# Kernel optimization log

Measured on AMD Instinct MI355X. Metric: run time of the kernel, lower is better.

## Reference

```python
import jax, jax.numpy as jnp
import numpy as np

N_NODES = 100000
N_EDGES = 1600000
D = 64
BN_EPS = 1e-5


def setup_inputs() -> dict:
    key = jax.random.key(0)
    ks = jax.random.split(key, 10)
    s = 1.0 / np.sqrt(D)
    return {
        "features": jax.random.normal(ks[0], (N_NODES, D), dtype=jnp.float32),
        "src": jax.random.randint(ks[1], (N_EDGES,), 0, N_NODES, dtype=jnp.int32),
        "dst": jax.random.randint(ks[2], (N_EDGES,), 0, N_NODES, dtype=jnp.int32),
        "eps": jnp.zeros((), dtype=jnp.float32),
        "W1": jax.random.uniform(ks[3], (D, D), jnp.float32, -s, s),
        "b1": jax.random.uniform(ks[4], (D,), jnp.float32, -s, s),
        "W2": jax.random.uniform(ks[5], (D, D), jnp.float32, -s, s),
        "b2": jax.random.uniform(ks[6], (D,), jnp.float32, -s, s),
        "gamma": jnp.ones((D,), dtype=jnp.float32),
        "beta": jnp.zeros((D,), dtype=jnp.float32),
    }


def reference(features, src, dst, eps, W1, b1, W2, b2, gamma, beta):
    h_in = features
    # message passing: gather src node features, scatter-sum to dst (fn.copy_u + fn.sum)
    neigh = jax.ops.segment_sum(features[src], dst, num_segments=N_NODES)  # [N, D]
    # eps-weighted self term
    h = (1.0 + eps) * features + neigh
    # apply_func MLP: Linear -> ReLU -> Linear
    h = jnp.maximum(h @ W1 + b1, 0.0) @ W2 + b2
    # BatchNorm1d over nodes (training-mode batch statistics)
    mean = jnp.mean(h, axis=0)
    var = jnp.var(h, axis=0)
    h = (h - mean) * jax.lax.rsqrt(var + BN_EPS) * gamma + beta
    # activation
    h = jnp.maximum(h, 0.0)
    # residual (indim == outdim)
    h = h_in + h
    # dropout p=0 -> identity
    return h
```

## Files before the change

kernel.cpp:

```cpp
#include <hip/hip_runtime.h>
#include <hip/hip_fp16.h>

#define N_NODES 100000
#define N_EDGES 1600000
#define D 64
#define BN_EPS 1e-5f
#define NBKT 256
#define NPB 391
#define BKT_CAP 7680
#define SORT_T 1024
#define NSHARD 64

typedef _Float16 half8 __attribute__((ext_vector_type(8)));
typedef float f32x4 __attribute__((ext_vector_type(4)));

__global__ __launch_bounds__(256) void bucket_k(
    const int* __restrict__ src, const int* __restrict__ dst,
    int* __restrict__ bkt_cnt, int2* __restrict__ bktbuf)
{
    __shared__ int h[NBKT], base[NBKT], cur[NBKT];
    const int t = threadIdx.x;
    if (t < NBKT) { h[t] = 0; cur[t] = 0; }
    __syncthreads();
    const int e0 = blockIdx.x * 4096;
    int s[16], d[16], b[16];
    #pragma unroll
    for (int i = 0; i < 16; ++i) {
        int e = e0 + i * 256 + t;
        if (e < N_EDGES) {
            s[i] = src[e];
            d[i] = dst[e];
            b[i] = d[i] / NPB;
            atomicAdd(&h[b[i]], 1);
        } else {
            b[i] = -1;
        }
    }
    __syncthreads();
    if (t < NBKT) base[t] = atomicAdd(&bkt_cnt[t], h[t]);
    __syncthreads();
    #pragma unroll
    for (int i = 0; i < 16; ++i) {
        if (b[i] >= 0) {
            int p = atomicAdd(&cur[b[i]], 1);
            bktbuf[(size_t)b[i] * BKT_CAP + base[b[i]] + p] = make_int2(s[i], d[i]);
        }
    }
}

__global__ __launch_bounds__(SORT_T) void sort_k(
    const int2* __restrict__ bktbuf, const int* __restrict__ bkt_cnt,
    int* __restrict__ rowptr, int* __restrict__ col)
{
    __shared__ int h[NPB];
    __shared__ int cur[NPB];
    __shared__ int part[SORT_T];
    __shared__ int bsc[NBKT];

    const int b = blockIdx.x;
    const int t = threadIdx.x;
    const int nb0 = b * NPB;
    const int nodes_in = min(NPB, N_NODES - nb0);
    const int cnt = bkt_cnt[b];
    const int2* buf = bktbuf + (size_t)b * BKT_CAP;

    if (t < NBKT) bsc[t] = bkt_cnt[t];
    __syncthreads();
    for (int off = 1; off < NBKT; off <<= 1) {
        int x = 0;
        if (t < NBKT) {
            x = bsc[t];
            if (t >= off) x += bsc[t - off];
        }
        __syncthreads();
        if (t < NBKT) bsc[t] = x;
        __syncthreads();
    }
    const int gbase = bsc[b] - cnt;

    if (t < NPB) h[t] = 0;
    __syncthreads();

    for (int i = t; i < cnt; i += SORT_T)
        atomicAdd(&h[buf[i].y - nb0], 1);
    __syncthreads();

    int a = (t < NPB) ? h[t] : 0;
    part[t] = a;
    __syncthreads();
    for (int off = 1; off < SORT_T; off <<= 1) {
        int x = part[t];
        int u = (t >= off) ? part[t - off] : 0;
        __syncthreads();
        part[t] = x + u;
        __syncthreads();
    }
    int excl = part[t] - a;
    if (t < NPB) {
        cur[t] = excl;
        if (t < nodes_in) rowptr[nb0 + t] = gbase + excl;
    }
    if (b == NBKT - 1 && t == 0) rowptr[N_NODES] = N_EDGES;
    __syncthreads();

    for (int i = t; i < cnt; i += SORT_T) {
        int2 r = buf[i];
        int slot = atomicAdd(&cur[r.y - nb0], 1);
        col[gbase + slot] = r.x;
    }
}

__global__ __launch_bounds__(256) void conv_k(
    const float* __restrict__ feat, __half* __restrict__ feat16)
{
    size_t i = ((size_t)blockIdx.x * 256 + threadIdx.x) * 8;
    if (i < (size_t)N_NODES * D) {
        float4 v0 = *(const float4*)(feat + i);
        float4 v1 = *(const float4*)(feat + i + 4);
        __half2 o[4];
        o[0] = __floats2half2_rn(v0.x, v0.y);
        o[1] = __floats2half2_rn(v0.z, v0.w);
        o[2] = __floats2half2_rn(v1.x, v1.y);
        o[3] = __floats2half2_rn(v1.z, v1.w);
        *(float4*)(feat16 + i) = *(float4*)o;
    }
}

__global__ __launch_bounds__(256) void wprep_k(
    const float* __restrict__ W1, const float* __restrict__ W2,
    _Float16* __restrict__ w1t, _Float16* __restrict__ w2t)
{
    const int t = threadIdx.x;
    const int n = t >> 2;
    const int k0 = (t & 3) * 16;
    _Float16 o1[16], o2[16];
    #pragma unroll
    for (int j = 0; j < 16; ++j) {
        o1[j] = (_Float16)W1[(k0 + j) * 64 + n];
        o2[j] = (_Float16)W2[(k0 + j) * 64 + n];
    }
    #pragma unroll
    for (int j = 0; j < 16; j += 8) {
        *(half8*)(w1t + n * 64 + k0 + j) = *(half8*)&o1[j];
        *(half8*)(w2t + n * 64 + k0 + j) = *(half8*)&o2[j];
    }
}

__global__ __launch_bounds__(256) void gather16_k(
    const __half* __restrict__ feat16, const int* __restrict__ rowptr,
    const int* __restrict__ col, const float* __restrict__ epsp,
    __half* __restrict__ x16)
{
    int node = blockIdx.x * 4 + (threadIdx.x >> 6);
    int lane = threadIdx.x & 63;
    if (node >= N_NODES) return;
    int g = lane >> 3;
    int c = (lane & 7) << 3;
    int lo = rowptr[node];
    int hi = rowptr[node + 1];
    float a[8] = {0.f, 0.f, 0.f, 0.f, 0.f, 0.f, 0.f, 0.f};
    int e = lo + g;
    for (; e + 8 < hi; e += 16) {
        int s0 = col[e];
        int s1 = col[e + 8];
        float4 r0 = *(const float4*)(feat16 + (size_t)s0 * D + c);
        float4 r1 = *(const float4*)(feat16 + (size_t)s1 * D + c);
        const __half2* h0 = (const __half2*)&r0;
        const __half2* h1 = (const __half2*)&r1;
        #pragma unroll
        for (int i = 0; i < 4; ++i) {
            float2 f0 = __half22float2(h0[i]);
            float2 f1 = __half22float2(h1[i]);
            a[2 * i]     += f0.x + f1.x;
            a[2 * i + 1] += f0.y + f1.y;
        }
    }
    if (e < hi) {
        float4 r0 = *(const float4*)(feat16 + (size_t)col[e] * D + c);
        const __half2* h0 = (const __half2*)&r0;
        #pragma unroll
        for (int i = 0; i < 4; ++i) {
            float2 f0 = __half22float2(h0[i]);
            a[2 * i]     += f0.x;
            a[2 * i + 1] += f0.y;
        }
    }
    #pragma unroll
    for (int off = 8; off <= 32; off <<= 1)
        #pragma unroll
        for (int i = 0; i < 8; ++i)
            a[i] += __shfl_xor(a[i], off, 64);
    if (g == 0) {
        float4 rs = *(const float4*)(feat16 + (size_t)node * D + c);
        const __half2* hs = (const __half2*)&rs;
        const float epsv = 1.0f + epsp[0];
        __half2 o[4];
        #pragma unroll
        for (int i = 0; i < 4; ++i) {
            float2 fs = __half22float2(hs[i]);
            o[i] = __floats2half2_rn(fmaf(epsv, fs.x, a[2 * i]),
                                     fmaf(epsv, fs.y, a[2 * i + 1]));
        }
        *(float4*)(x16 + (size_t)node * D + c) = *(float4*)o;
    }
}

__global__ __launch_bounds__(256) void gather32_k(
    const float* __restrict__ feat, const int* __restrict__ rowptr,
    const int* __restrict__ col, const float* __restrict__ epsp,
    float* __restrict__ x)
{
    int node = blockIdx.x * 4 + (threadIdx.x >> 6);
    int lane = threadIdx.x & 63;
    if (node >= N_NODES) return;
    int g = lane >> 4;
    int c = (lane & 15) << 2;
    int lo = rowptr[node];
    int hi = rowptr[node + 1];
    float ax = 0.f, ay = 0.f, az = 0.f, aw = 0.f;
    int e = lo + g;
    for (; e + 4 < hi; e += 8) {
        int s0 = col[e];
        int s1 = col[e + 4];
        float4 v0 = *(const float4*)(feat + (size_t)s0 * D + c);
        float4 v1 = *(const float4*)(feat + (size_t)s1 * D + c);
        ax += v0.x; ay += v0.y; az += v0.z; aw += v0.w;
        ax += v1.x; ay += v1.y; az += v1.z; aw += v1.w;
    }
    if (e < hi) {
        float4 v = *(const float4*)(feat + (size_t)col[e] * D + c);
        ax += v.x; ay += v.y; az += v.z; aw += v.w;
    }
    #pragma unroll
    for (int off = 16; off <= 32; off <<= 1) {
        ax += __shfl_xor(ax, off, 64);
        ay += __shfl_xor(ay, off, 64);
        az += __shfl_xor(az, off, 64);
        aw += __shfl_xor(aw, off, 64);
    }
    if (g == 0) {
        float4 f = *(const float4*)(feat + (size_t)node * D + c);
        const float epsv = 1.0f + epsp[0];
        float4 r;
        r.x = fmaf(epsv, f.x, ax);
        r.y = fmaf(epsv, f.y, ay);
        r.z = fmaf(epsv, f.z, az);
        r.w = fmaf(epsv, f.w, aw);
        *(float4*)(x + (size_t)node * D + c) = r;
    }
}

__global__ __launch_bounds__(256) void mfma_mlp2_k(
    const __half* __restrict__ x16,
    const _Float16* __restrict__ w1t, const _Float16* __restrict__ w2t,
    const float* __restrict__ b1, const float* __restrict__ b2,
    __half* __restrict__ h216, float* __restrict__ stats)
{
    __shared__ __align__(16) _Float16 xts[64 * 72];

    const int t    = threadIdx.x;
    const int w    = t >> 6;
    const int lane = t & 63;
    const int m    = lane & 15;
    const int q    = lane >> 4;
    const int rbase = w * 16;
    const int nb   = blockIdx.x * 64;

    const _Float16* xg = (const _Float16*)x16 + (size_t)(nb + rbase + m) * 64 + q * 8;
    half8 a0 = *(const half8*)(xg);
    half8 a1 = *(const half8*)(xg + 32);

    f32x4 acc[4];
    #pragma unroll
    for (int jt = 0; jt < 4; ++jt) {
        const float bias = b1[jt * 16 + m];
        acc[jt] = (f32x4){bias, bias, bias, bias};
        const _Float16* bw = w1t + (jt * 16 + m) * 64 + q * 8;
        half8 bf0 = *(const half8*)(bw);
        half8 bf1 = *(const half8*)(bw + 32);
        acc[jt] = __builtin_amdgcn_mfma_f32_16x16x32_f16(a0, bf0, acc[jt], 0, 0, 0);
        acc[jt] = __builtin_amdgcn_mfma_f32_16x16x32_f16(a1, bf1, acc[jt], 0, 0, 0);
    }

    #pragma unroll
    for (int jt = 0; jt < 4; ++jt)
        #pragma unroll
        for (int r = 0; r < 4; ++r)
            xts[(rbase + q * 4 + r) * 72 + jt * 16 + m] =
                (_Float16)fmaxf(acc[jt][r], 0.0f);
    asm volatile("s_waitcnt lgkmcnt(0)" ::: "memory");

    const _Float16* xw = &xts[(rbase + m) * 72 + q * 8];
    half8 c0 = *(const half8*)(xw);
    half8 c1 = *(const half8*)(xw + 32);

    f32x4 acc2[4];
    #pragma unroll
    for (int jt = 0; jt < 4; ++jt) {
        const float bias = b2[jt * 16 + m];
        acc2[jt] = (f32x4){bias, bias, bias, bias};
        const _Float16* bw = w2t + (jt * 16 + m) * 64 + q * 8;
        half8 bf0 = *(const half8*)(bw);
        half8 bf1 = *(const half8*)(bw + 32);
        acc2[jt] = __builtin_amdgcn_mfma_f32_16x16x32_f16(c0, bf0, acc2[jt], 0, 0, 0);
        acc2[jt] = __builtin_amdgcn_mfma_f32_16x16x32_f16(c1, bf1, acc2[jt], 0, 0, 0);
    }
    asm volatile("s_waitcnt lgkmcnt(0)" ::: "memory");

    float psums[4], psqs[4];
    #pragma unroll
    for (int jt = 0; jt < 4; ++jt) {
        float ps = 0.f, pq = 0.f;
        #pragma unroll
        for (int r = 0; r < 4; ++r) {
            const int row = rbase + q * 4 + r;
            const float v = acc2[jt][r];
            const float vv = (nb + row < N_NODES) ? v : 0.f;
            ps += vv;
            pq += vv * vv;
            xts[row * 72 + jt * 16 + m] = (_Float16)v;
        }
        ps += __shfl_xor(ps, 16, 64); ps += __shfl_xor(ps, 32, 64);
        pq += __shfl_xor(pq, 16, 64); pq += __shfl_xor(pq, 32, 64);
        psums[jt] = ps; psqs[jt] = pq;
    }
    if (lane < 16) {
        float* sp = stats + (size_t)(blockIdx.x & (NSHARD - 1)) * 128;
        #pragma unroll
        for (int jt = 0; jt < 4; ++jt) {
            unsafeAtomicAdd(sp + jt * 16 + lane,      psums[jt]);
            unsafeAtomicAdd(sp + 64 + jt * 16 + lane, psqs[jt]);
        }
    }
    asm volatile("s_waitcnt lgkmcnt(0)" ::: "memory");

    {
        const int rr = lane >> 2;
        const int cc = (lane & 3) * 16;
        const int gn = nb + rbase + rr;
        if (gn < N_NODES) {
            float4 r0 = *(const float4*)&xts[(rbase + rr) * 72 + cc];
            float4 r1 = *(const float4*)&xts[(rbase + rr) * 72 + cc + 8];
            *(float4*)(h216 + (size_t)gn * 64 + cc)     = r0;
            *(float4*)(h216 + (size_t)gn * 64 + cc + 8) = r1;
        }
    }
}

__global__ __launch_bounds__(256) void mlp32_k(
    const float* __restrict__ x,
    const float* __restrict__ W1, const float* __restrict__ b1,
    const float* __restrict__ W2, const float* __restrict__ b2,
    float* __restrict__ h2out, float* __restrict__ stats)
{
    __shared__ float W1s[64 * 68];
    __shared__ float W2s[64 * 68];
    __shared__ float xs[64 * 65];
    __shared__ float b1s[64], b2s[64];

    const int t  = threadIdx.x;
    const int nb = blockIdx.x * 64;

    #pragma unroll
    for (int i = 0; i < 4; ++i) {
        int l  = t + i * 256;
        int k  = l >> 4;
        int j4 = (l & 15) << 2;
        *(float4*)(&W1s[k * 68 + j4]) = *(const float4*)(W1 + k * 64 + j4);
        *(float4*)(&W2s[k * 68 + j4]) = *(const float4*)(W2 + k * 64 + j4);
    }
    if (t < 64)       b1s[t]      = b1[t];
    else if (t < 128) b2s[t - 64] = b2[t - 64];

    #pragma unroll
    for (int i = 0; i < 2; ++i) {
        int n  = (t >> 3) + i * 32;
        int k8 = (t & 7) << 3;
        int gn = nb + n;
        float4 a = make_float4(0.f, 0.f, 0.f, 0.f), b = a;
        if (gn < N_NODES) {
            a = *(const float4*)(x + (size_t)gn * D + k8);
            b = *(const float4*)(x + (size_t)gn * D + k8 + 4);
        }
        *(float4*)&xs[n * 65 + k8]     = a;
        *(float4*)&xs[n * 65 + k8 + 4] = b;
    }
    __syncthreads();

    const int n0 = (t & 15) << 2;
    const int j0 = (t >> 4) << 2;
    const float* xr0 = &xs[(n0 + 0) * 65];
    const float* xr1 = &xs[(n0 + 1) * 65];
    const float* xr2 = &xs[(n0 + 2) * 65];
    const float* xr3 = &xs[(n0 + 3) * 65];

    float acc[4][4];
    #pragma unroll
    for (int a = 0; a < 4; ++a)
        #pragma unroll
        for (int b = 0; b < 4; ++b)
            acc[a][b] = b1s[j0 + b];

    #pragma unroll 8
    for (int k = 0; k < 64; ++k) {
        const float4 w = *(const float4*)(&W1s[k * 68 + j0]);
        const float x0 = xr0[k], x1 = xr1[k], x2 = xr2[k], x3 = xr3[k];
        acc[0][0] = fmaf(x0, w.x, acc[0][0]); acc[0][1] = fmaf(x0, w.y, acc[0][1]);
        acc[0][2] = fmaf(x0, w.z, acc[0][2]); acc[0][3] = fmaf(x0, w.w, acc[0][3]);
        acc[1][0] = fmaf(x1, w.x, acc[1][0]); acc[1][1] = fmaf(x1, w.y, acc[1][1]);
        acc[1][2] = fmaf(x1, w.z, acc[1][2]); acc[1][3] = fmaf(x1, w.w, acc[1][3]);
        acc[2][0] = fmaf(x2, w.x, acc[2][0]); acc[2][1] = fmaf(x2, w.y, acc[2][1]);
        acc[2][2] = fmaf(x2, w.z, acc[2][2]); acc[2][3] = fmaf(x2, w.w, acc[2][3]);
        acc[3][0] = fmaf(x3, w.x, acc[3][0]); acc[3][1] = fmaf(x3, w.y, acc[3][1]);
        acc[3][2] = fmaf(x3, w.z, acc[3][2]); acc[3][3] = fmaf(x3, w.w, acc[3][3]);
    }

    __syncthreads();
    #pragma unroll
    for (int a = 0; a < 4; ++a)
        #pragma unroll
        for (int b = 0; b < 4; ++b)
            xs[(n0 + a) * 65 + j0 + b] = fmaxf(acc[a][b], 0.0f);
    __syncthreads();

    float acc2[4][4];
    #pragma unroll
    for (int a = 0; a < 4; ++a)
        #pragma unroll
        for (int b = 0; b < 4; ++b)
            acc2[a][b] = b2s[j0 + b];

    #pragma unroll 8
    for (int k = 0; k < 64; ++k) {
        const float4 w = *(const float4*)(&W2s[k * 68 + j0]);
        const float x0 = xr0[k], x1 = xr1[k], x2 = xr2[k], x3 = xr3[k];
        acc2[0][0] = fmaf(x0, w.x, acc2[0][0]); acc2[0][1] = fmaf(x0, w.y, acc2[0][1]);
        acc2[0][2] = fmaf(x0, w.z, acc2[0][2]); acc2[0][3] = fmaf(x0, w.w, acc2[0][3]);
        acc2[1][0] = fmaf(x1, w.x, acc2[1][0]); acc2[1][1] = fmaf(x1, w.y, acc2[1][1]);
        acc2[1][2] = fmaf(x1, w.z, acc2[1][2]); acc2[1][3] = fmaf(x1, w.w, acc2[1][3]);
        acc2[2][0] = fmaf(x2, w.x, acc2[2][0]); acc2[2][1] = fmaf(x2, w.y, acc2[2][1]);
        acc2[2][2] = fmaf(x2, w.z, acc2[2][2]); acc2[2][3] = fmaf(x2, w.w, acc2[2][3]);
        acc2[3][0] = fmaf(x3, w.x, acc2[3][0]); acc2[3][1] = fmaf(x3, w.y, acc2[3][1]);
        acc2[3][2] = fmaf(x3, w.z, acc2[3][2]); acc2[3][3] = fmaf(x3, w.w, acc2[3][3]);
    }

    float psum[4] = {0.f, 0.f, 0.f, 0.f};
    float psq[4]  = {0.f, 0.f, 0.f, 0.f};
    #pragma unroll
    for (int a = 0; a < 4; ++a) {
        int gn = nb + n0 + a;
        if (gn < N_NODES) {
            float4 hh;
            hh.x = acc2[a][0]; hh.y = acc2[a][1]; hh.z = acc2[a][2]; hh.w = acc2[a][3];
            *(float4*)(h2out + (size_t)gn * 64 + j0) = hh;
            psum[0] += hh.x; psq[0] += hh.x * hh.x;
            psum[1] += hh.y; psq[1] += hh.y * hh.y;
            psum[2] += hh.z; psq[2] += hh.z * hh.z;
            psum[3] += hh.w; psq[3] += hh.w * hh.w;
        }
    }
    #pragma unroll
    for (int off = 8; off >= 1; off >>= 1)
        #pragma unroll
        for (int b = 0; b < 4; ++b) {
            psum[b] += __shfl_down(psum[b], off, 16);
            psq[b]  += __shfl_down(psq[b],  off, 16);
        }
    if ((t & 15) == 0) {
        float* sp = stats + (size_t)(blockIdx.x & (NSHARD - 1)) * 128;
        #pragma unroll
        for (int b = 0; b < 4; ++b) {
            unsafeAtomicAdd(sp + j0 + b,      psum[b]);
            unsafeAtomicAdd(sp + 64 + j0 + b, psq[b]);
        }
    }
}

__global__ void bnstats_k(const float* __restrict__ stats,
                          const float* __restrict__ gamma,
                          const float* __restrict__ beta,
                          float* __restrict__ sf)
{
    int j = threadIdx.x;
    float s = 0.f, q = 0.f;
    for (int c = 0; c < NSHARD; ++c) {
        s += stats[c * 128 + j];
        q += stats[c * 128 + 64 + j];
    }
    const float invN = 1.0f / (float)N_NODES;
    float mean  = s * invN;
    float var   = q * invN - mean * mean;
    float scale = gamma[j] * rsqrtf(var + BN_EPS);
    sf[j]      = scale;
    sf[64 + j] = beta[j] - mean * scale;
}

__global__ __launch_bounds__(256) void finish16_k(
    const float* __restrict__ feat, const __half* __restrict__ h216,
    const float* __restrict__ sf, float* __restrict__ out)
{
    __shared__ float scs[64], shs[64];
    if (threadIdx.x < 64) {
        scs[threadIdx.x] = sf[threadIdx.x];
        shs[threadIdx.x] = sf[64 + threadIdx.x];
    }
    __syncthreads();
    size_t i = (size_t)blockIdx.x * 256 + threadIdx.x;
    if (i < (size_t)N_NODES * D / 4) {
        int j = (int)((i * 4) & 63);
        const __half2* hp = (const __half2*)(h216 + i * 4);
        float2 h0 = __half22float2(hp[0]);
        float2 h1 = __half22float2(hp[1]);
        float4 f = *(const float4*)(feat + i * 4);
        float4 o;
        o.x = fmaxf(fmaf(h0.x, scs[j + 0], shs[j + 0]), 0.f) + f.x;
        o.y = fmaxf(fmaf(h0.y, scs[j + 1], shs[j + 1]), 0.f) + f.y;
        o.z = fmaxf(fmaf(h1.x, scs[j + 2], shs[j + 2]), 0.f) + f.z;
        o.w = fmaxf(fmaf(h1.y, scs[j + 3], shs[j + 3]), 0.f) + f.w;
        *(float4*)(out + i * 4) = o;
    }
}

__global__ __launch_bounds__(256) void finish_k(
    const float* __restrict__ feat, const float* __restrict__ sf,
    float* __restrict__ out)
{
    __shared__ float scs[64], shs[64];
    if (threadIdx.x < 64) {
        scs[threadIdx.x] = sf[threadIdx.x];
        shs[threadIdx.x] = sf[64 + threadIdx.x];
    }
    __syncthreads();
    size_t i = (size_t)blockIdx.x * 256 + threadIdx.x;
    if (i < (size_t)N_NODES * D / 4) {
        int j = (int)((i * 4) & 63);
        float4 h = *(float4*)(out + i * 4);
        float4 f = *(const float4*)(feat + i * 4);
        h.x = fmaxf(fmaf(h.x, scs[j + 0], shs[j + 0]), 0.f) + f.x;
        h.y = fmaxf(fmaf(h.y, scs[j + 1], shs[j + 1]), 0.f) + f.y;
        h.z = fmaxf(fmaf(h.z, scs[j + 2], shs[j + 2]), 0.f) + f.z;
        h.w = fmaxf(fmaf(h.w, scs[j + 3], shs[j + 3]), 0.f) + f.w;
        *(float4*)(out + i * 4) = h;
    }
}

extern "C" void kernel_launch(void* const* d_in, const int* in_sizes, int n_in,
                              void* d_out, int out_size, void* d_ws, size_t ws_size,
                              hipStream_t stream)
{
    const float* feat  = (const float*)d_in[0];
    const int*   src   = (const int*)d_in[1];
    const int*   dst   = (const int*)d_in[2];
    const float* eps   = (const float*)d_in[3];
    const float* W1    = (const float*)d_in[4];
    const float* b1    = (const float*)d_in[5];
    const float* W2    = (const float*)d_in[6];
    const float* b2    = (const float*)d_in[7];
    const float* gamma = (const float*)d_in[8];
    const float* beta  = (const float*)d_in[9];
    float* out = (float*)d_out;

    const size_t BKTSZ = (size_t)NBKT * BKT_CAP * sizeof(int2);
    const size_t F16SZ = (size_t)N_NODES * D * sizeof(__half);
    const size_t X32SZ = (size_t)N_NODES * D * sizeof(float);
    const size_t COLSZ = (size_t)N_EDGES * sizeof(int);
    const size_t RPSZ  = (size_t)(N_NODES + 1) * sizeof(int);
    const size_t STATSZ = (size_t)NSHARD * 128 * sizeof(float);
    const size_t TAIL  = STATSZ + NBKT * 4 + 128 * 4 + 2 * 4096 * sizeof(_Float16) + 256;
    const size_t need16 = BKTSZ + F16SZ + COLSZ + RPSZ + TAIL;

    if (ws_size >= need16) {
        char* p = (char*)d_ws;
        __half* x16    = (__half*)p;
        int2*   bktbuf = (int2*)p;
        __half* feat16 = (__half*)(p + BKTSZ);
        __half* h216   = (__half*)(p + BKTSZ);
        int*    col    = (int*)(p + BKTSZ + F16SZ);
        int*    rowptr = col + N_EDGES;
        float*  stats  = (float*)(rowptr + N_NODES + 1);
        int*    bkt_cnt = (int*)(stats + NSHARD * 128);
        float*  sf     = (float*)(bkt_cnt + NBKT);
        _Float16* w1t  = (_Float16*)(sf + 128);
        _Float16* w2t  = w1t + 4096;

        hipMemsetAsync(stats, 0, STATSZ + NBKT * 4, stream);
        conv_k<<<3125, 256, 0, stream>>>(feat, feat16);
        wprep_k<<<1, 256, 0, stream>>>(W1, W2, w1t, w2t);
        bucket_k<<<(N_EDGES + 4095) / 4096, 256, 0, stream>>>(src, dst, bkt_cnt, bktbuf);
        sort_k<<<NBKT, SORT_T, 0, stream>>>(bktbuf, bkt_cnt, rowptr, col);
        gather16_k<<<(N_NODES + 3) / 4, 256, 0, stream>>>(feat16, rowptr, col, eps, x16);
        mfma_mlp2_k<<<(N_NODES + 63) / 64, 256, 0, stream>>>(x16, w1t, w2t, b1, b2, h216, stats);
        bnstats_k<<<1, 64, 0, stream>>>(stats, gamma, beta, sf);
        finish16_k<<<(N_NODES * D / 4 + 255) / 256, 256, 0, stream>>>(feat, h216, sf, out);
    } else {
        char* p = (char*)d_ws;
        float* x32    = (float*)p;
        int2*  bktbuf = (int2*)p;
        int*   col    = (int*)(p + X32SZ);
        int*   rowptr = col + N_EDGES;
        float* stats  = (float*)(rowptr + N_NODES + 1);
        int*   bkt_cnt = (int*)(stats + NSHARD * 128);
        float* sf     = (float*)(bkt_cnt + NBKT);

        hipMemsetAsync(stats, 0, STATSZ + NBKT * 4, stream);
        bucket_k<<<(N_EDGES + 4095) / 4096, 256, 0, stream>>>(src, dst, bkt_cnt, bktbuf);
        sort_k<<<NBKT, SORT_T, 0, stream>>>(bktbuf, bkt_cnt, rowptr, col);
        gather32_k<<<(N_NODES + 3) / 4, 256, 0, stream>>>(feat, rowptr, col, eps, x32);
        mlp32_k<<<(N_NODES + 63) / 64, 256, 0, stream>>>(x32, W1, b1, W2, b2, out, stats);
        bnstats_k<<<1, 64, 0, stream>>>(stats, gamma, beta, sf);
        finish_k<<<(N_NODES * D / 4 + 255) / 256, 256, 0, stream>>>(feat, sf, out);
    }
}
```

Before: 220.7 us.

## Fuse neighbor gather into MFMA MLP kernel and merge weight prep into conversion

The fp16 gather now runs inside the MLP kernel. Each wave gathers its 16 nodes straight into shared memory, so the x16 intermediate no longer makes a round trip through global memory and one launch is gone. Neighbor accumulation switches from fp32 to packed half2 adds, including the cross-lane reduction. This roughly halves the ALU work but raises rounding error and overflow risk for high-degree nodes. The weight transpose is folded into the feature conversion kernel as an extra block, and the MLP grid has fewer blocks with each wave processing nodes serially, which may reduce latency hiding in the gather.

```diff
diff --git a/kernel.cpp b/kernel.cpp
--- a/kernel.cpp
+++ b/kernel.cpp
@@ -14,6 +14,12 @@
 typedef _Float16 half8 __attribute__((ext_vector_type(8)));
 typedef float f32x4 __attribute__((ext_vector_type(4)));
 
+__device__ inline __half2 shflx2(__half2 v, int off) {
+    int iv = *(int*)&v;
+    iv = __shfl_xor(iv, off, 64);
+    return *(__half2*)&iv;
+}
+
 __global__ __launch_bounds__(256) void bucket_k(
     const int* __restrict__ src, const int* __restrict__ dst,
     int* __restrict__ bkt_cnt, int2* __restrict__ bktbuf)
@@ -111,10 +117,12 @@
 }
 
 __global__ __launch_bounds__(256) void conv_k(
-    const float* __restrict__ feat, __half* __restrict__ feat16)
-{
-    size_t i = ((size_t)blockIdx.x * 256 + threadIdx.x) * 8;
-    if (i < (size_t)N_NODES * D) {
+    const float* __restrict__ feat, __half* __restrict__ feat16,
+    const float* __restrict__ W1, const float* __restrict__ W2,
+    _Float16* __restrict__ w1t, _Float16* __restrict__ w2t)
+{
+    if (blockIdx.x < 3125) {
+        size_t i = ((size_t)blockIdx.x * 256 + threadIdx.x) * 8;
         float4 v0 = *(const float4*)(feat + i);
         float4 v1 = *(const float4*)(feat + i + 4);
         __half2 o[4];
@@ -123,85 +131,180 @@
         o[2] = __floats2half2_rn(v1.x, v1.y);
         o[3] = __floats2half2_rn(v1.z, v1.w);
         *(float4*)(feat16 + i) = *(float4*)o;
-    }
-}
-
-__global__ __launch_bounds__(256) void wprep_k(
-    const float* __restrict__ W1, const float* __restrict__ W2,
-    _Float16* __restrict__ w1t, _Float16* __restrict__ w2t)
-{
-    const int t = threadIdx.x;
-    const int n = t >> 2;
-    const int k0 = (t & 3) * 16;
-    _Float16 o1[16], o2[16];
-    #pragma unroll
-    for (int j = 0; j < 16; ++j) {
-        o1[j] = (_Float16)W1[(k0 + j) * 64 + n];
-        o2[j] = (_Float16)W2[(k0 + j) * 64 + n];
-    }
-    #pragma unroll
-    for (int j = 0; j < 16; j += 8) {
-        *(half8*)(w1t + n * 64 + k0 + j) = *(half8*)&o1[j];
-        *(half8*)(w2t + n * 64 + k0 + j) = *(half8*)&o2[j];
-    }
-}
-
-__global__ __launch_bounds__(256) void gather16_k(
+    } else {
+        const int t = threadIdx.x;
+        const int n = t >> 2;
+        const int k0 = (t & 3) * 16;
+        _Float16 o1[16], o2[16];
+        #pragma unroll
+        for (int j = 0; j < 16; ++j) {
+            o1[j] = (_Float16)W1[(k0 + j) * 64 + n];
+            o2[j] = (_Float16)W2[(k0 + j) * 64 + n];
+        }
+        #pragma unroll
+        for (int j = 0; j < 16; j += 8) {
+            *(half8*)(w1t + n * 64 + k0 + j) = *(half8*)&o1[j];
+            *(half8*)(w2t + n * 64 + k0 + j) = *(half8*)&o2[j];
+        }
+    }
+}
+
+__global__ __launch_bounds__(256) void gmlp_k(
     const __half* __restrict__ feat16, const int* __restrict__ rowptr,
     const int* __restrict__ col, const float* __restrict__ epsp,
-    __half* __restrict__ x16)
-{
-    int node = blockIdx.x * 4 + (threadIdx.x >> 6);
-    int lane = threadIdx.x & 63;
-    if (node >= N_NODES) return;
-    int g = lane >> 3;
-    int c = (lane & 7) << 3;
-    int lo = rowptr[node];
-    int hi = rowptr[node + 1];
-    float a[8] = {0.f, 0.f, 0.f, 0.f, 0.f, 0.f, 0.f, 0.f};
-    int e = lo + g;
-    for (; e + 8 < hi; e += 16) {
-        int s0 = col[e];
-        int s1 = col[e + 8];
-        float4 r0 = *(const float4*)(feat16 + (size_t)s0 * D + c);
-        float4 r1 = *(const float4*)(feat16 + (size_t)s1 * D + c);
-        const __half2* h0 = (const __half2*)&r0;
-        const __half2* h1 = (const __half2*)&r1;
-        #pragma unroll
-        for (int i = 0; i < 4; ++i) {
-            float2 f0 = __half22float2(h0[i]);
-            float2 f1 = __half22float2(h1[i]);
-            a[2 * i]     += f0.x + f1.x;
-            a[2 * i + 1] += f0.y + f1.y;
-        }
-    }
-    if (e < hi) {
-        float4 r0 = *(const float4*)(feat16 + (size_t)col[e] * D + c);
-        const __half2* h0 = (const __half2*)&r0;
-        #pragma unroll
-        for (int i = 0; i < 4; ++i) {
-            float2 f0 = __half22float2(h0[i]);
-            a[2 * i]     += f0.x;
-            a[2 * i + 1] += f0.y;
-        }
-    }
-    #pragma unroll
-    for (int off = 8; off <= 32; off <<= 1)
-        #pragma unroll
-        for (int i = 0; i < 8; ++i)
-            a[i] += __shfl_xor(a[i], off, 64);
-    if (g == 0) {
-        float4 rs = *(const float4*)(feat16 + (size_t)node * D + c);
-        const __half2* hs = (const __half2*)&rs;
-        const float epsv = 1.0f + epsp[0];
-        __half2 o[4];
-        #pragma unroll
-        for (int i = 0; i < 4; ++i) {
-            float2 fs = __half22float2(hs[i]);
-            o[i] = __floats2half2_rn(fmaf(epsv, fs.x, a[2 * i]),
-                                     fmaf(epsv, fs.y, a[2 * i + 1]));
-        }
-        *(float4*)(x16 + (size_t)node * D + c) = *(float4*)o;
+    const _Float16* __restrict__ w1t, const _Float16* __restrict__ w2t,
+    const float* __restrict__ b1, const float* __restrict__ b2,
+    __half* __restrict__ h216, float* __restrict__ stats)
+{
+    __shared__ __align__(16) _Float16 xts[64 * 72];
+
+    const int t     = threadIdx.x;
+    const int w     = t >> 6;
+    const int lane  = t & 63;
+    const int rbase = w * 16;
+    const int nb    = blockIdx.x * 64;
+    const int gn0   = nb + rbase;
+
+    const float epsv = 1.0f + epsp[0];
+    const __half2 epsh = __float2half2_rn(epsv);
+
+    int rp = 0;
+    if (lane < 17 && gn0 + lane <= N_NODES) rp = rowptr[gn0 + lane];
+
+    const int g = lane >> 3;
+    const int c = (lane & 7) << 3;
+
+    for (int i = 0; i < 16; ++i) {
+        const int gn = gn0 + i;
+        if (gn >= N_NODES) {
+            if (g == 0) {
+                float4 z = make_float4(0.f, 0.f, 0.f, 0.f);
+                *(float4*)&xts[(rbase + i) * 72 + c] = z;
+            }
+            continue;
+        }
+        const int lo = __shfl(rp, i, 64);
+        const int hi = __shfl(rp, i + 1, 64);
+        __half2 a0 = __float2half2_rn(0.f), a1 = a0, a2 = a0, a3 = a0;
+        int e = lo + g;
+        for (; e + 8 < hi; e += 16) {
+            int s0 = col[e];
+            int s1 = col[e + 8];
+            float4 r0 = *(const float4*)(feat16 + (size_t)s0 * D + c);
+            float4 r1 = *(const float4*)(feat16 + (size_t)s1 * D + c);
+            const __half2* h0 = (const __half2*)&r0;
+            const __half2* h1 = (const __half2*)&r1;
+            a0 = __hadd2(a0, h0[0]); a1 = __hadd2(a1, h0[1]);
+            a2 = __hadd2(a2, h0[2]); a3 = __hadd2(a3, h0[3]);
+            a0 = __hadd2(a0, h1[0]); a1 = __hadd2(a1, h1[1]);
+            a2 = __hadd2(a2, h1[2]); a3 = __hadd2(a3, h1[3]);
+        }
+        if (e < hi) {
+            float4 r0 = *(const float4*)(feat16 + (size_t)col[e] * D + c);
+            const __half2* h0 = (const __half2*)&r0;
+            a0 = __hadd2(a0, h0[0]); a1 = __hadd2(a1, h0[1]);
+            a2 = __hadd2(a2, h0[2]); a3 = __hadd2(a3, h0[3]);
+        }
+        #pragma unroll
+        for (int off = 8; off <= 32; off <<= 1) {
+            a0 = __hadd2(a0, shflx2(a0, off));
+            a1 = __hadd2(a1, shflx2(a1, off));
+            a2 = __hadd2(a2, shflx2(a2, off));
+            a3 = __hadd2(a3, shflx2(a3, off));
+        }
+        if (g == 0) {
+            float4 rs = *(const float4*)(feat16 + (size_t)gn * D + c);
+            const __half2* hs = (const __half2*)&rs;
+            __half2 o[4];
+            o[0] = __hfma2(epsh, hs[0], a0);
+            o[1] = __hfma2(epsh, hs[1], a1);
+            o[2] = __hfma2(epsh, hs[2], a2);
+            o[3] = __hfma2(epsh, hs[3], a3);
+            *(float4*)&xts[(rbase + i) * 72 + c] = *(float4*)o;
+        }
+    }
+    asm volatile("s_waitcnt lgkmcnt(0)" ::: "memory");
+
+    const int m = lane & 15;
+    const int q = lane >> 4;
+
+    const _Float16* xw = &xts[(rbase + m) * 72 + q * 8];
+    half8 a0 = *(const half8*)(xw);
+    half8 a1 = *(const half8*)(xw + 32);
+
+    f32x4 acc[4];
+    #pragma unroll
+    for (int jt = 0; jt < 4; ++jt) {
+        const float bias = b1[jt * 16 + m];
+        acc[jt] = (f32x4){bias, bias, bias, bias};
+        const _Float16* bw = w1t + (jt * 16 + m) * 64 + q * 8;
+        half8 bf0 = *(const half8*)(bw);
+        half8 bf1 = *(const half8*)(bw + 32);
+        acc[jt] = __builtin_amdgcn_mfma_f32_16x16x32_f16(a0, bf0, acc[jt], 0, 0, 0);
+        acc[jt] = __builtin_amdgcn_mfma_f32_16x16x32_f16(a1, bf1, acc[jt], 0, 0, 0);
+    }
+
+    #pragma unroll
+    for (int jt = 0; jt < 4; ++jt)
+        #pragma unroll
+        for (int r = 0; r < 4; ++r)
+            xts[(rbase + q * 4 + r) * 72 + jt * 16 + m] =
+                (_Float16)fmaxf(acc[jt][r], 0.0f);
+    asm volatile("s_waitcnt lgkmcnt(0)" ::: "memory");
+
+    half8 c0 = *(const half8*)(xw);
+    half8 c1 = *(const half8*)(xw + 32);
+
+    f32x4 acc2[4];
+    #pragma unroll
+    for (int jt = 0; jt < 4; ++jt) {
+        const float bias = b2[jt * 16 + m];
+        acc2[jt] = (f32x4){bias, bias, bias, bias};
+        const _Float16* bw = w2t + (jt * 16 + m) * 64 + q * 8;
+        half8 bf0 = *(const half8*)(bw);
+        half8 bf1 = *(const half8*)(bw + 32);
+        acc2[jt] = __builtin_amdgcn_mfma_f32_16x16x32_f16(c0, bf0, acc2[jt], 0, 0, 0);
+        acc2[jt] = __builtin_amdgcn_mfma_f32_16x16x32_f16(c1, bf1, acc2[jt], 0, 0, 0);
+    }
+    asm volatile("s_waitcnt lgkmcnt(0)" ::: "memory");
+
+    float psums[4], psqs[4];
+    #pragma unroll
+    for (int jt = 0; jt < 4; ++jt) {
+        float ps = 0.f, pq = 0.f;
+        #pragma unroll
+        for (int r = 0; r < 4; ++r) {
+            const int row = rbase + q * 4 + r;
+            const float v = acc2[jt][r];
+            const float vv = (nb + row < N_NODES) ? v : 0.f;
+            ps += vv;
+            pq += vv * vv;
+            xts[row * 72 + jt * 16 + m] = (_Float16)v;
+        }
+        ps += __shfl_xor(ps, 16, 64); ps += __shfl_xor(ps, 32, 64);
+        pq += __shfl_xor(pq, 16, 64); pq += __shfl_xor(pq, 32, 64);
+        psums[jt] = ps; psqs[jt] = pq;
+    }
+    if (lane < 16) {
+        float* sp = stats + (size_t)(blockIdx.x & (NSHARD - 1)) * 128;
+        #pragma unroll
+        for (int jt = 0; jt < 4; ++jt) {
+            unsafeAtomicAdd(sp + jt * 16 + lane,      psums[jt]);
+            unsafeAtomicAdd(sp + 64 + jt * 16 + lane, psqs[jt]);
+        }
+    }
+    asm volatile("s_waitcnt lgkmcnt(0)" ::: "memory");
+
+    {
+        const int rr = lane >> 2;
+        const int cc = (lane & 3) * 16;
+        const int gn = nb + rbase + rr;
+        if (gn < N_NODES) {
+            float4 r0 = *(const float4*)&xts[(rbase + rr) * 72 + cc];
+            float4 r1 = *(const float4*)&xts[(rbase + rr) * 72 + cc + 8];
+            *(float4*)(h216 + (size_t)gn * 64 + cc)     = r0;
+            *(float4*)(h216 + (size_t)gn * 64 + cc + 8) = r1;
+        }
     }
 }
 
@@ -250,103 +353,6 @@
     }
 }
 
-__global__ __launch_bounds__(256) void mfma_mlp2_k(
-    const __half* __restrict__ x16,
-    const _Float16* __restrict__ w1t, const _Float16* __restrict__ w2t,
-    const float* __restrict__ b1, const float* __restrict__ b2,
-    __half* __restrict__ h216, float* __restrict__ stats)
-{
-    __shared__ __align__(16) _Float16 xts[64 * 72];
-
-    const int t    = threadIdx.x;
-    const int w    = t >> 6;
-    const int lane = t & 63;
-    const int m    = lane & 15;
-    const int q    = lane >> 4;
-    const int rbase = w * 16;
-    const int nb   = blockIdx.x * 64;
-
-    const _Float16* xg = (const _Float16*)x16 + (size_t)(nb + rbase + m) * 64 + q * 8;
-    half8 a0 = *(const half8*)(xg);
-    half8 a1 = *(const half8*)(xg + 32);
-
-    f32x4 acc[4];
-    #pragma unroll
-    for (int jt = 0; jt < 4; ++jt) {
-        const float bias = b1[jt * 16 + m];
-        acc[jt] = (f32x4){bias, bias, bias, bias};
-        const _Float16* bw = w1t + (jt * 16 + m) * 64 + q * 8;
-        half8 bf0 = *(const half8*)(bw);
-        half8 bf1 = *(const half8*)(bw + 32);
-        acc[jt] = __builtin_amdgcn_mfma_f32_16x16x32_f16(a0, bf0, acc[jt], 0, 0, 0);
-        acc[jt] = __builtin_amdgcn_mfma_f32_16x16x32_f16(a1, bf1, acc[jt], 0, 0, 0);
-    }
-
-    #pragma unroll
-    for (int jt = 0; jt < 4; ++jt)
-        #pragma unroll
-        for (int r = 0; r < 4; ++r)
-            xts[(rbase + q * 4 + r) * 72 + jt * 16 + m] =
-                (_Float16)fmaxf(acc[jt][r], 0.0f);
-    asm volatile("s_waitcnt lgkmcnt(0)" ::: "memory");
-
-    const _Float16* xw = &xts[(rbase + m) * 72 + q * 8];
-    half8 c0 = *(const half8*)(xw);
-    half8 c1 = *(const half8*)(xw + 32);
-
-    f32x4 acc2[4];
-    #pragma unroll
-    for (int jt = 0; jt < 4; ++jt) {
-        const float bias = b2[jt * 16 + m];
-        acc2[jt] = (f32x4){bias, bias, bias, bias};
-        const _Float16* bw = w2t + (jt * 16 + m) * 64 + q * 8;
-        half8 bf0 = *(const half8*)(bw);
-        half8 bf1 = *(const half8*)(bw + 32);
-        acc2[jt] = __builtin_amdgcn_mfma_f32_16x16x32_f16(c0, bf0, acc2[jt], 0, 0, 0);
-        acc2[jt] = __builtin_amdgcn_mfma_f32_16x16x32_f16(c1, bf1, acc2[jt], 0, 0, 0);
-    }
-    asm volatile("s_waitcnt lgkmcnt(0)" ::: "memory");
-
-    float psums[4], psqs[4];
-    #pragma unroll
-    for (int jt = 0; jt < 4; ++jt) {
-        float ps = 0.f, pq = 0.f;
-        #pragma unroll
-        for (int r = 0; r < 4; ++r) {
-            const int row = rbase + q * 4 + r;
-            const float v = acc2[jt][r];
-            const float vv = (nb + row < N_NODES) ? v : 0.f;
-            ps += vv;
-            pq += vv * vv;
-            xts[row * 72 + jt * 16 + m] = (_Float16)v;
-        }
-        ps += __shfl_xor(ps, 16, 64); ps += __shfl_xor(ps, 32, 64);
-        pq += __shfl_xor(pq, 16, 64); pq += __shfl_xor(pq, 32, 64);
-        psums[jt] = ps; psqs[jt] = pq;
-    }
-    if (lane < 16) {
-        float* sp = stats + (size_t)(blockIdx.x & (NSHARD - 1)) * 128;
-        #pragma unroll
-        for (int jt = 0; jt < 4; ++jt) {
-            unsafeAtomicAdd(sp + jt * 16 + lane,      psums[jt]);
-            unsafeAtomicAdd(sp + 64 + jt * 16 + lane, psqs[jt]);
-        }
-    }
-    asm volatile("s_waitcnt lgkmcnt(0)" ::: "memory");
-
-    {
-        const int rr = lane >> 2;
-        const int cc = (lane & 3) * 16;
-        const int gn = nb + rbase + rr;
-        if (gn < N_NODES) {
-            float4 r0 = *(const float4*)&xts[(rbase + rr) * 72 + cc];
-            float4 r1 = *(const float4*)&xts[(rbase + rr) * 72 + cc + 8];
-            *(float4*)(h216 + (size_t)gn * 64 + cc)     = r0;
-            *(float4*)(h216 + (size_t)gn * 64 + cc + 8) = r1;
-        }
-    }
-}
-
 __global__ __launch_bounds__(256) void mlp32_k(
     const float* __restrict__ x,
     const float* __restrict__ W1, const float* __restrict__ b1,
@@ -571,10 +577,9 @@
 
     if (ws_size >= need16) {
         char* p = (char*)d_ws;
-        __half* x16    = (__half*)p;
         int2*   bktbuf = (int2*)p;
+        __half* h216   = (__half*)p;
         __half* feat16 = (__half*)(p + BKTSZ);
-        __half* h216   = (__half*)(p + BKTSZ);
         int*    col    = (int*)(p + BKTSZ + F16SZ);
         int*    rowptr = col + N_EDGES;
         float*  stats  = (float*)(rowptr + N_NODES + 1);
@@ -584,12 +589,11 @@
         _Float16* w2t  = w1t + 4096;
 
         hipMemsetAsync(stats, 0, STATSZ + NBKT * 4, stream);
-        conv_k<<<3125, 256, 0, stream>>>(feat, feat16);
-        wprep_k<<<1, 256, 0, stream>>>(W1, W2, w1t, w2t);
         bucket_k<<<(N_EDGES + 4095) / 4096, 256, 0, stream>>>(src, dst, bkt_cnt, bktbuf);
+        conv_k<<<3126, 256, 0, stream>>>(feat, feat16, W1, W2, w1t, w2t);
         sort_k<<<NBKT, SORT_T, 0, stream>>>(bktbuf, bkt_cnt, rowptr, col);
-        gather16_k<<<(N_NODES + 3) / 4, 256, 0, stream>>>(feat16, rowptr, col, eps, x16);
-        mfma_mlp2_k<<<(N_NODES + 63) / 64, 256, 0, stream>>>(x16, w1t, w2t, b1, b2, h216, stats);
+        gmlp_k<<<(N_NODES + 63) / 64, 256, 0, stream>>>(feat16, rowptr, col, eps,
+                                                        w1t, w2t, b1, b2, h216, stats);
         bnstats_k<<<1, 64, 0, stream>>>(stats, gamma, beta, sf);
         finish16_k<<<(N_NODES * D / 4 + 255) / 256, 256, 0, stream>>>(feat, h216, sf, out);
     } else {
```

Result: slower. 226.8 us (+2.7%).
